# Performance work log

Measured on AMD Instinct MI355X. Metric: run time of the kernel, lower is better.

## Reference

```python
import jax, jax.numpy as jnp
import numpy as np
from jax import lax

TEMP = 0.05
MOMENTUM = 0.9
EPS = 1e-12


def _l2_normalize(x, axis=-1):
    n = jnp.sqrt(jnp.sum(x * x, axis=axis, keepdims=True))
    return x / jnp.maximum(n, EPS)


def _cross_entropy(logits, targets):
    # mean over batch of -log_softmax(logits)[target]
    logp = jax.nn.log_softmax(logits, axis=-1)
    return -jnp.mean(jnp.take_along_axis(logp, targets[:, None], axis=-1))


def _momentum_update(features, x, targets, m):
    # Sequential per-sample read-modify-write (faithful to the torch loop,
    # matters when targets contain duplicates). carry = memory bank.
    def step(f, xy):
        x_i, y_i = xy
        row = m * f[y_i] + (1.0 - m) * x_i
        row = row / jnp.linalg.norm(row)
        return f.at[y_i].set(row), None
    f, _ = lax.scan(step, features, (x, targets))
    return f


def setup_inputs() -> dict:
    key = jax.random.key(0)
    k1, k2, k3, k4, k5, k6 = jax.random.split(key, 6)
    B, D, N = 512, 1024, 16384
    inputs_rgb = jax.random.normal(k1, (B, D), dtype=jnp.float32)
    inputs_ir = jax.random.normal(k2, (B, D), dtype=jnp.float32)
    targets_rgb = jax.random.randint(k3, (B,), 0, N, dtype=jnp.int32)
    targets_ir = jax.random.randint(k4, (B,), 0, N, dtype=jnp.int32)
    # memory banks (buffers); initialized as normalized random rows to mimic a
    # warmed-up cluster memory (the module starts at zeros, degenerate for CE)
    features_rgb = _l2_normalize(jax.random.normal(k5, (N, D), dtype=jnp.float32))
    features_ir = _l2_normalize(jax.random.normal(k6, (N, D), dtype=jnp.float32))
    return {"inputs_rgb": inputs_rgb, "inputs_ir": inputs_ir,
            "targets_rgb": targets_rgb, "targets_ir": targets_ir,
            "features_rgb": features_rgb, "features_ir": features_ir}


def reference(inputs_rgb, inputs_ir, targets_rgb, targets_ir, features_rgb, features_ir):
    x_rgb = _l2_normalize(inputs_rgb)  # [B, D]
    x_ir = _l2_normalize(inputs_ir)
    logits_rgb = (x_rgb @ features_rgb.T) / TEMP  # [B, N]
    logits_ir = (x_ir @ features_ir.T) / TEMP
    loss_rgb = _cross_entropy(logits_rgb, targets_rgb)
    loss_ir = _cross_entropy(logits_ir, targets_ir)
    # side-effect of CM.backward in the original: momentum scatter update + renorm
    # (change_scale == 1.0 so the Hungarian cross-modal exchange is skipped)
    new_features_rgb = _momentum_update(features_rgb, x_rgb, targets_rgb, MOMENTUM)
    new_features_ir = _momentum_update(features_ir, x_ir, targets_ir, MOMENTUM)
    return (loss_rgb, loss_ir, new_features_rgb, new_features_ir)
```

## Files before the change

kernel.cpp:

```cpp
#include <hip/hip_runtime.h>
#include <math.h>

#define BATCH 512
#define DIM   1024
#define NCLUS 16384
#define TINV  20.0f

typedef __attribute__((ext_vector_type(4))) float f32x4;
typedef __attribute__((ext_vector_type(8))) short bf16x8;

static __device__ __forceinline__ unsigned short f2bf(float f) {
  unsigned int u = __float_as_uint(f);
  u += 0x7FFFu + ((u >> 16) & 1u);
  return (unsigned short)(u >> 16);
}

__global__ void nrm_kernel(const float* __restrict__ in_rgb,
                           const float* __restrict__ in_ir,
                           float* __restrict__ xf,
                           unsigned short* __restrict__ xb,
                           float* __restrict__ accum) {
  int gid = blockIdx.x * blockDim.x + threadIdx.x;
  if (gid < 2048) accum[gid] = 0.0f;

  int row = blockIdx.x;
  int mod = row >> 9;
  int r   = row & 511;
  const float* in = (mod ? in_ir : in_rgb) + (size_t)r * DIM;
  float* xo          = xf + ((size_t)mod * BATCH + r) * DIM;
  unsigned short* xbo = xb + ((size_t)mod * BATCH + r) * DIM;

  int t = threadIdx.x;
  float4 v = ((const float4*)in)[t];
  float ss = v.x*v.x + v.y*v.y + v.z*v.z + v.w*v.w;
#pragma unroll
  for (int m = 1; m < 64; m <<= 1) ss += __shfl_xor(ss, m, 64);
  __shared__ float red[4];
  if ((t & 63) == 0) red[t >> 6] = ss;
  __syncthreads();
  float inv = 1.0f / fmaxf(sqrtf(red[0] + red[1] + red[2] + red[3]), 1e-12f);
  float4 o = make_float4(v.x * inv, v.y * inv, v.z * inv, v.w * inv);
  ((float4*)xo)[t] = o;
  ushort4 ob = make_ushort4(f2bf(o.x), f2bf(o.y), f2bf(o.z), f2bf(o.w));
  ((ushort4*)xbo)[t] = ob;
}

#define BM 128
#define BN 128
#define BK 32
#define LDP 40

__global__ void gemm_lse_kernel(const unsigned short* __restrict__ xb,
                                const float* __restrict__ f_rgb,
                                const float* __restrict__ f_ir,
                                const int* __restrict__ t_rgb,
                                const int* __restrict__ t_ir,
                                float* __restrict__ rowsum,
                                float* __restrict__ tgtlog) {
  const int mod = blockIdx.y;
  const unsigned short* X = xb + (size_t)mod * BATCH * DIM;
  const float* F  = mod ? f_ir : f_rgb;
  const int*   tg = mod ? t_ir : t_rgb;
  float* rs = rowsum + mod * BATCH;
  float* tl = tgtlog + mod * BATCH;

  const int nt = blockIdx.x >> 2;
  const int bt = blockIdx.x & 3;

  __shared__ unsigned short As[BM][LDP];
  __shared__ unsigned short Bs[BN][LDP];

  const int tid  = threadIdx.x;
  const int wid  = tid >> 6;
  const int lane = tid & 63;
  const int wr = wid >> 1, wc = wid & 1;
  const int l15 = lane & 15, lhi = lane >> 4;

  f32x4 acc[4][4];
#pragma unroll
  for (int m = 0; m < 4; ++m)
#pragma unroll
    for (int n = 0; n < 4; ++n) acc[m][n] = (f32x4){0.f, 0.f, 0.f, 0.f};

  for (int kk = 0; kk < DIM; kk += BK) {
#pragma unroll
    for (int i = 0; i < 2; ++i) {
      int id = tid + i * 256;
      int row = id >> 2, c8 = (id & 3) << 3;
      uint4 v = *(const uint4*)(X + (size_t)(bt * BM + row) * DIM + kk + c8);
      *(uint4*)(&As[row][c8]) = v;
    }
#pragma unroll
    for (int i = 0; i < 4; ++i) {
      int id = tid + i * 256;
      int row = id >> 3, c4 = (id & 7) << 2;
      float4 v = *(const float4*)(F + (size_t)(nt * BN + row) * DIM + kk + c4);
      ushort4 b = make_ushort4(f2bf(v.x), f2bf(v.y), f2bf(v.z), f2bf(v.w));
      *(ushort4*)(&Bs[row][c4]) = b;
    }
    __syncthreads();

    bf16x8 a[4], b[4];
#pragma unroll
    for (int m = 0; m < 4; ++m)
      a[m] = *(const bf16x8*)(&As[wr * 64 + m * 16 + l15][lhi * 8]);
#pragma unroll
    for (int n = 0; n < 4; ++n)
      b[n] = *(const bf16x8*)(&Bs[wc * 64 + n * 16 + l15][lhi * 8]);
#pragma unroll
    for (int m = 0; m < 4; ++m)
#pragma unroll
      for (int n = 0; n < 4; ++n)
        acc[m][n] = __builtin_amdgcn_mfma_f32_16x16x32_bf16(a[m], b[n], acc[m][n], 0, 0, 0);
    __syncthreads();
  }

#pragma unroll
  for (int m = 0; m < 4; ++m) {
    const int browbase = bt * BM + wr * 64 + m * 16 + lhi * 4;
    float esum[4];
#pragma unroll
    for (int j = 0; j < 4; ++j) {
      const int brow = browbase + j;
      const int t = tg[brow];
      float e = 0.f;
#pragma unroll
      for (int n = 0; n < 4; ++n) {
        float logit = acc[m][n][j] * TINV;
        e += __expf(logit);
        int col = nt * BN + wc * 64 + n * 16 + l15;
        if (col == t) tl[brow] = logit;
      }
      esum[j] = e;
    }
#pragma unroll
    for (int j = 0; j < 4; ++j) {
      float e = esum[j];
      e += __shfl_xor(e, 1, 64);
      e += __shfl_xor(e, 2, 64);
      e += __shfl_xor(e, 4, 64);
      e += __shfl_xor(e, 8, 64);
      if (l15 == 0) atomicAdd(rs + browbase + j, e);
    }
  }
}

__global__ void copy_kernel(const float* __restrict__ f_rgb,
                            const float* __restrict__ f_ir,
                            float* __restrict__ out) {
  const size_t n2 = (size_t)NCLUS * DIM / 2;
  size_t stride = (size_t)gridDim.x * blockDim.x;
  for (size_t i = (size_t)blockIdx.x * blockDim.x + threadIdx.x; i < 2 * n2; i += stride) {
    float2 v = (i < n2) ? ((const float2*)f_rgb)[i] : ((const float2*)f_ir)[i - n2];
    ((float2*)out)[i] = v;
  }
}

__global__ void loss_kernel(const float* __restrict__ rowsum,
                            const float* __restrict__ tgtlog,
                            float* __restrict__ out) {
  int t = threadIdx.x;
  float lr = logf(rowsum[t]) - tgtlog[t];
  float li = logf(rowsum[BATCH + t]) - tgtlog[BATCH + t];
#pragma unroll
  for (int m = 1; m < 64; m <<= 1) { lr += __shfl_xor(lr, m, 64); li += __shfl_xor(li, m, 64); }
  __shared__ float sr[8], si[8];
  if ((t & 63) == 0) { sr[t >> 6] = lr; si[t >> 6] = li; }
  __syncthreads();
  if (t == 0) {
    float a = 0.f, b = 0.f;
#pragma unroll
    for (int i = 0; i < 8; ++i) { a += sr[i]; b += si[i]; }
    out[0] = a * (1.0f / BATCH);
    out[1] = b * (1.0f / BATCH);
  }
}

__global__ void mom_kernel(const int* __restrict__ t_rgb,
                           const int* __restrict__ t_ir,
                           const float* __restrict__ xf,
                           float* __restrict__ out) {
  const int i   = blockIdx.x;
  const int mod = blockIdx.y;
  const int* tg = mod ? t_ir : t_rgb;
  const int y = tg[i];
  for (int j = 0; j < i; ++j)
    if (tg[j] == y) return;

  const float* x = xf + (size_t)mod * BATCH * DIM;
  float* rowp = out + (size_t)mod * NCLUS * DIM + (size_t)y * DIM;

  const int t = threadIdx.x;
  float2 r0 = ((const float2*)rowp)[t];
  float2 r1 = ((const float2*)rowp)[t + 256];
  __shared__ float red[4];

  for (int j = i; j < BATCH; ++j) {
    if (tg[j] != y) continue;
    const float2* xr = (const float2*)(x + (size_t)j * DIM);
    float2 x0 = xr[t], x1 = xr[t + 256];
    r0.x = 0.9f * r0.x + 0.1f * x0.x;
    r0.y = 0.9f * r0.y + 0.1f * x0.y;
    r1.x = 0.9f * r1.x + 0.1f * x1.x;
    r1.y = 0.9f * r1.y + 0.1f * x1.y;
    float ss = r0.x*r0.x + r0.y*r0.y + r1.x*r1.x + r1.y*r1.y;
#pragma unroll
    for (int m = 1; m < 64; m <<= 1) ss += __shfl_xor(ss, m, 64);
    if ((t & 63) == 0) red[t >> 6] = ss;
    __syncthreads();
    float tot = red[0] + red[1] + red[2] + red[3];
    __syncthreads();
    float inv = 1.0f / sqrtf(tot);
    r0.x *= inv; r0.y *= inv; r1.x *= inv; r1.y *= inv;
  }
  ((float2*)rowp)[t] = r0;
  ((float2*)rowp)[t + 256] = r1;
}

extern "C" void kernel_launch(void* const* d_in, const int* in_sizes, int n_in,
                              void* d_out, int out_size, void* d_ws, size_t ws_size,
                              hipStream_t stream) {
  (void)in_sizes; (void)n_in; (void)out_size; (void)ws_size;
  const float* in_rgb = (const float*)d_in[0];
  const float* in_ir  = (const float*)d_in[1];
  const int*   t_rgb  = (const int*)d_in[2];
  const int*   t_ir   = (const int*)d_in[3];
  const float* f_rgb  = (const float*)d_in[4];
  const float* f_ir   = (const float*)d_in[5];
  float* out = (float*)d_out;

  char* ws = (char*)d_ws;
  float*          xf     = (float*)ws;
  unsigned short* xb     = (unsigned short*)(ws + 4194304);
  float*          rowsum = (float*)(ws + 6291456);
  float*          tgtlog = rowsum + 1024;

  nrm_kernel<<<1024, 256, 0, stream>>>(in_rgb, in_ir, xf, xb, rowsum);
  gemm_lse_kernel<<<dim3(512, 2), 256, 0, stream>>>(xb, f_rgb, f_ir, t_rgb, t_ir, rowsum, tgtlog);
  copy_kernel<<<8192, 256, 0, stream>>>(f_rgb, f_ir, out + 2);
  loss_kernel<<<1, 512, 0, stream>>>(rowsum, tgtlog, out);
  mom_kernel<<<dim3(512, 2), 256, 0, stream>>>(t_rgb, t_ir, xf, out + 2);
}
```

Measured before the change: 202.4 us.

## Fuse bank copy with bf16 pre-conversion and stream GEMM tiles via global_load_lds

```diff
diff --git a/kernel.cpp b/kernel.cpp
--- a/kernel.cpp
+++ b/kernel.cpp
@@ -13,6 +13,12 @@
   unsigned int u = __float_as_uint(f);
   u += 0x7FFFu + ((u >> 16) & 1u);
   return (unsigned short)(u >> 16);
+}
+
+typedef const __attribute__((address_space(1))) unsigned int* gas1_t;
+typedef __attribute__((address_space(3))) unsigned int* las3_t;
+static __device__ __forceinline__ void gload16(const void* g, void* l) {
+  __builtin_amdgcn_global_load_lds((gas1_t)g, (las3_t)l, 16, 0, 0);
 }
 
 __global__ void nrm_kernel(const float* __restrict__ in_rgb,
@@ -45,30 +51,49 @@
   ((ushort4*)xbo)[t] = ob;
 }
 
+__global__ void cvtcopy_kernel(const float* __restrict__ f_rgb,
+                               const float* __restrict__ f_ir,
+                               float* __restrict__ out,
+                               unsigned short* __restrict__ fb,
+                               int precvt) {
+  const size_t n4 = (size_t)NCLUS * DIM / 4;
+  size_t stride = (size_t)gridDim.x * blockDim.x;
+  for (size_t i = (size_t)blockIdx.x * blockDim.x + threadIdx.x; i < 2 * n4; i += stride) {
+    const float4 v = (i < n4) ? ((const float4*)f_rgb)[i] : ((const float4*)f_ir)[i - n4];
+    float2* o2 = (float2*)(out + 4 * i);
+    o2[0] = make_float2(v.x, v.y);
+    o2[1] = make_float2(v.z, v.w);
+    if (precvt)
+      ((ushort4*)fb)[i] = make_ushort4(f2bf(v.x), f2bf(v.y), f2bf(v.z), f2bf(v.w));
+  }
+}
+
 #define BM 128
 #define BN 128
 #define BK 32
-#define LDP 40
-
+
+template<int PRECVT>
 __global__ void gemm_lse_kernel(const unsigned short* __restrict__ xb,
+                                const unsigned short* __restrict__ fb,
                                 const float* __restrict__ f_rgb,
                                 const float* __restrict__ f_ir,
                                 const int* __restrict__ t_rgb,
                                 const int* __restrict__ t_ir,
                                 float* __restrict__ rowsum,
                                 float* __restrict__ tgtlog) {
-  const int mod = blockIdx.y;
-  const unsigned short* X = xb + (size_t)mod * BATCH * DIM;
-  const float* F  = mod ? f_ir : f_rgb;
+  const int nt  = blockIdx.x;
+  const int bt  = blockIdx.y & 3;
+  const int mod = blockIdx.y >> 2;
+
+  const unsigned short* X  = xb + ((size_t)mod * BATCH + bt * BM) * DIM;
+  const unsigned short* Bb = fb + ((size_t)mod * NCLUS + nt * BN) * DIM;
+  const float* Ff = (mod ? f_ir : f_rgb) + (size_t)nt * BN * DIM;
   const int*   tg = mod ? t_ir : t_rgb;
   float* rs = rowsum + mod * BATCH;
   float* tl = tgtlog + mod * BATCH;
 
-  const int nt = blockIdx.x >> 2;
-  const int bt = blockIdx.x & 3;
-
-  __shared__ unsigned short As[BM][LDP];
-  __shared__ unsigned short Bs[BN][LDP];
+  __shared__ __align__(16) unsigned short As[BM * BK];
+  __shared__ __align__(16) unsigned short Bs[BN * BK];
 
   const int tid  = threadIdx.x;
   const int wid  = tid >> 6;
@@ -85,28 +110,32 @@
   for (int kk = 0; kk < DIM; kk += BK) {
 #pragma unroll
     for (int i = 0; i < 2; ++i) {
-      int id = tid + i * 256;
-      int row = id >> 2, c8 = (id & 3) << 3;
-      uint4 v = *(const uint4*)(X + (size_t)(bt * BM + row) * DIM + kk + c8);
-      *(uint4*)(&As[row][c8]) = v;
-    }
-#pragma unroll
-    for (int i = 0; i < 4; ++i) {
-      int id = tid + i * 256;
-      int row = id >> 3, c4 = (id & 7) << 2;
-      float4 v = *(const float4*)(F + (size_t)(nt * BN + row) * DIM + kk + c4);
-      ushort4 b = make_ushort4(f2bf(v.x), f2bf(v.y), f2bf(v.z), f2bf(v.w));
-      *(ushort4*)(&Bs[row][c4]) = b;
+      int q = i * 256 + tid;
+      gload16(X + (size_t)(q >> 2) * DIM + kk + (q & 3) * 8,
+              As + (size_t)(i * 256 + wid * 64) * 8);
+      if (PRECVT)
+        gload16(Bb + (size_t)(q >> 2) * DIM + kk + (q & 3) * 8,
+                Bs + (size_t)(i * 256 + wid * 64) * 8);
+    }
+    if (!PRECVT) {
+#pragma unroll
+      for (int i = 0; i < 4; ++i) {
+        int id = i * 256 + tid;
+        int row = id >> 3, c4 = (id & 7) << 2;
+        float4 v = *(const float4*)(Ff + (size_t)row * DIM + kk + c4);
+        *(ushort4*)(&Bs[row * BK + c4]) =
+            make_ushort4(f2bf(v.x), f2bf(v.y), f2bf(v.z), f2bf(v.w));
+      }
     }
     __syncthreads();
 
     bf16x8 a[4], b[4];
 #pragma unroll
     for (int m = 0; m < 4; ++m)
-      a[m] = *(const bf16x8*)(&As[wr * 64 + m * 16 + l15][lhi * 8]);
+      a[m] = *(const bf16x8*)(&As[(wr * 64 + m * 16 + l15) * BK + lhi * 8]);
 #pragma unroll
     for (int n = 0; n < 4; ++n)
-      b[n] = *(const bf16x8*)(&Bs[wc * 64 + n * 16 + l15][lhi * 8]);
+      b[n] = *(const bf16x8*)(&Bs[(wc * 64 + n * 16 + l15) * BK + lhi * 8]);
 #pragma unroll
     for (int m = 0; m < 4; ++m)
 #pragma unroll
@@ -142,17 +171,6 @@
       e += __shfl_xor(e, 8, 64);
       if (l15 == 0) atomicAdd(rs + browbase + j, e);
     }
-  }
-}
-
-__global__ void copy_kernel(const float* __restrict__ f_rgb,
-                            const float* __restrict__ f_ir,
-                            float* __restrict__ out) {
-  const size_t n2 = (size_t)NCLUS * DIM / 2;
-  size_t stride = (size_t)gridDim.x * blockDim.x;
-  for (size_t i = (size_t)blockIdx.x * blockDim.x + threadIdx.x; i < 2 * n2; i += stride) {
-    float2 v = (i < n2) ? ((const float2*)f_rgb)[i] : ((const float2*)f_ir)[i - n2];
-    ((float2*)out)[i] = v;
   }
 }
 
@@ -220,7 +238,7 @@
 extern "C" void kernel_launch(void* const* d_in, const int* in_sizes, int n_in,
                               void* d_out, int out_size, void* d_ws, size_t ws_size,
                               hipStream_t stream) {
-  (void)in_sizes; (void)n_in; (void)out_size; (void)ws_size;
+  (void)in_sizes; (void)n_in; (void)out_size;
   const float* in_rgb = (const float*)d_in[0];
   const float* in_ir  = (const float*)d_in[1];
   const int*   t_rgb  = (const int*)d_in[2];
@@ -231,13 +249,20 @@
 
   char* ws = (char*)d_ws;
   float*          xf     = (float*)ws;
-  unsigned short* xb     = (unsigned short*)(ws + 4194304);
-  float*          rowsum = (float*)(ws + 6291456);
+  unsigned short* xb     = (unsigned short*)(ws + (4u<<20));
+  float*          rowsum = (float*)(ws + (6u<<20));
   float*          tgtlog = rowsum + 1024;
+  unsigned short* fb     = (unsigned short*)(ws + (8u<<20));
+  const int precvt = (ws_size >= ((size_t)72 << 20)) ? 1 : 0;
 
   nrm_kernel<<<1024, 256, 0, stream>>>(in_rgb, in_ir, xf, xb, rowsum);
-  gemm_lse_kernel<<<dim3(512, 2), 256, 0, stream>>>(xb, f_rgb, f_ir, t_rgb, t_ir, rowsum, tgtlog);
-  copy_kernel<<<8192, 256, 0, stream>>>(f_rgb, f_ir, out + 2);
+  cvtcopy_kernel<<<2048, 256, 0, stream>>>(f_rgb, f_ir, out + 2, fb, precvt);
+  if (precvt)
+    gemm_lse_kernel<1><<<dim3(128, 8), 256, 0, stream>>>(xb, fb, f_rgb, f_ir,
+                                                         t_rgb, t_ir, rowsum, tgtlog);
+  else
+    gemm_lse_kernel<0><<<dim3(128, 8), 256, 0, stream>>>(xb, fb, f_rgb, f_ir,
+                                                         t_rgb, t_ir, rowsum, tgtlog);
+  mom_kernel<<<dim3(512, 2), 256, 0, stream>>>(t_rgb, t_ir, xf, out + 2);
   loss_kernel<<<1, 512, 0, stream>>>(rowsum, tgtlog, out);
-  mom_kernel<<<dim3(512, 2), 256, 0, stream>>>(t_rgb, t_ir, xf, out + 2);
-}
+}
```

Result: faster. 189.5 us (-6.4%).
